# Kernel tuning notes

Hardware: AMD Instinct MI355X
Metric: run time of the kernel (lower is better)

## Reference

```python
import jax, jax.numpy as jnp
import numpy as np

EMB_DIM = 300
VOCAB_X = 50000
VOCAB_Y = 50000
LEN_X = 64
LEN_Y = 64
BATCH = 1024
PAD_ID = 0


def setup_inputs() -> dict:
    key = jax.random.key(0)
    k1, k2, k3, k4, k5, k6, k7 = jax.random.split(key, 7)
    initrange = 0.5 / EMB_DIM
    emb_x = jax.random.uniform(k1, (VOCAB_X, EMB_DIM), jnp.float32, -initrange, initrange)
    emb_y = jax.random.uniform(k2, (VOCAB_Y, EMB_DIM), jnp.float32, -initrange, initrange)
    # padding row zeroed as in init_emb
    emb_x = emb_x.at[PAD_ID].set(0.0)
    emb_y = emb_y.at[PAD_ID].set(0.0)
    return {
        "samp_hid": jax.random.normal(k3, (BATCH, EMB_DIM), jnp.float32),
        "batch_x": jax.random.randint(k4, (BATCH, LEN_X), 0, VOCAB_X, jnp.int64 if jax.config.jax_enable_x64 else jnp.int32),
        "batch_y": jax.random.randint(k5, (BATCH, LEN_Y), 0, VOCAB_Y, jnp.int64 if jax.config.jax_enable_x64 else jnp.int32),
        "emb_x": emb_x,
        "emb_y": emb_y,
        "bias_x": jax.random.uniform(k6, (VOCAB_X,), jnp.float32),
        "bias_y": jax.random.uniform(k7, (VOCAB_Y,), jnp.float32),
    }


def _cal_nll(z, tokens, emb, bias):
    # logits shared across all positions: [B, V]
    logits = z @ emb.T + bias
    logp = jax.nn.log_softmax(logits, axis=-1)            # compute log-softmax ONCE per row
    tok_logp = jnp.take_along_axis(logp, tokens, axis=1)  # [B, L] gather per-position targets
    mask = (tokens != PAD_ID).astype(logits.dtype)        # CrossEntropyLoss(ignore_index=0)
    return jnp.sum(-tok_logp * mask, axis=1)              # sum over positions -> [B]


def reference(samp_hid, batch_x, batch_y, emb_x, emb_y, bias_x, bias_y):
    nll_x = _cal_nll(samp_hid, batch_x, emb_x, bias_x)
    nll_y = _cal_nll(samp_hid, batch_y, emb_y, bias_y)
    return jnp.mean(nll_x + nll_y)
```

## Files before the change

kernel.cpp:

```cpp
#include <hip/hip_runtime.h>

#define V_VOCAB 50000
#define K_DIM   300
#define NROWS   1024
#define LEN     64
#define NBC     98
#define CGS     784
#define KS      19

typedef __attribute__((ext_vector_type(8)))  short bf16x8;
typedef __attribute__((ext_vector_type(16))) float f32x16;

static __device__ __forceinline__ unsigned short f2bf(float f) {
    unsigned int u = __builtin_bit_cast(unsigned int, f);
    u = u + 0x7fffu + ((u >> 16) & 1u);
    return (unsigned short)(u >> 16);
}

static __device__ __forceinline__ f32x16 zero16() {
    f32x16 z;
#pragma unroll
    for (int i = 0; i < 16; ++i) z[i] = 0.0f;
    return z;
}

__global__ void zbf_kernel(const float* __restrict__ z, unsigned short* __restrict__ zbf) {
    int t = blockIdx.x * 256 + threadIdx.x;
    int l    = t & 63;
    int rest = t >> 6;
    int ks   = rest % KS;
    int rblk = rest / KS;
    int row  = rblk * 32 + (l & 31);
    int k0   = ks * 16 + (l >> 5) * 8;
    unsigned short o[8];
#pragma unroll
    for (int j = 0; j < 8; ++j) {
        int k = k0 + j;
        float v = (k < K_DIM) ? z[row * K_DIM + k] : ((k == K_DIM) ? 1.0f : 0.0f);
        o[j] = f2bf(v);
    }
    ushort4* p = (ushort4*)(zbf + (size_t)t * 8);
    p[0] = make_ushort4(o[0], o[1], o[2], o[3]);
    p[1] = make_ushort4(o[4], o[5], o[6], o[7]);
}

__launch_bounds__(512, 2)
__global__ void gemm_kernel(const unsigned short* __restrict__ zbf,
                            const float* __restrict__ emb_x,
                            const float* __restrict__ emb_y,
                            const float* __restrict__ bias_x,
                            const float* __restrict__ bias_y,
                            float* __restrict__ partial) {
    __shared__ unsigned short Zs[2][19456];

    const int tid  = threadIdx.x;
    const int lane = tid & 63;
    const int w    = tid >> 6;
    const int side = blockIdx.y;
    const int bc   = blockIdx.x;
    const float* eg = side ? emb_y : emb_x;
    const float* bg = side ? bias_y : bias_x;
    const int c0 = bc * 512 + w * 64;

    bf16x8 a[2][KS];
#pragma unroll
    for (int cb = 0; cb < 2; ++cb) {
        const int c = c0 + cb * 32 + (lane & 31);
        const bool cv = (c < V_VOCAB);
        const float* erow = eg + (size_t)c * K_DIM;
        const int khi = (lane >> 5) * 8;
#pragma unroll
        for (int ks = 0; ks < KS; ++ks) {
            const int k0 = ks * 16 + khi;
            float f[8];
            if (k0 + 8 <= K_DIM) {
                float4 u  = cv ? *(const float4*)(erow + k0)     : make_float4(0, 0, 0, 0);
                float4 v2 = cv ? *(const float4*)(erow + k0 + 4) : make_float4(0, 0, 0, 0);
                f[0] = u.x;  f[1] = u.y;  f[2] = u.z;  f[3] = u.w;
                f[4] = v2.x; f[5] = v2.y; f[6] = v2.z; f[7] = v2.w;
            } else {
#pragma unroll
                for (int j = 0; j < 8; ++j) {
                    int k = k0 + j;
                    f[j] = (k < K_DIM) ? (cv ? erow[k] : 0.0f)
                         : (k == K_DIM ? (cv ? bg[c] : -3e38f) : 0.0f);
                }
            }
            bf16x8 t;
#pragma unroll
            for (int j = 0; j < 8; ++j) t[j] = (short)f2bf(f[j]);
            a[cb][ks] = t;
        }
    }

    const int cg = (side * NBC + bc) * 8 + w;
    float* pout = partial + (size_t)cg * NROWS;

    uint4 st[5];
    {
        const uint4* src = (const uint4*)zbf;
#pragma unroll
        for (int i = 0; i < 5; ++i) { int idx = i * 512 + tid; if (idx < 2432) st[i] = src[idx]; }
        uint4* dst = (uint4*)&Zs[0][0];
#pragma unroll
        for (int i = 0; i < 5; ++i) { int idx = i * 512 + tid; if (idx < 2432) dst[i * 512 + tid] = st[i]; }
    }
    __syncthreads();

    int buf = 0;
    for (int p = 0; p < 16; ++p) {
        if (p < 15) {
            const uint4* src = (const uint4*)(zbf + (size_t)(p + 1) * 19456);
#pragma unroll
            for (int i = 0; i < 5; ++i) { int idx = i * 512 + tid; if (idx < 2432) st[i] = src[idx]; }
        }

        const unsigned short* zb = &Zs[buf][0];
        f32x16 acc00 = zero16(), acc01 = zero16(), acc10 = zero16(), acc11 = zero16();
#pragma unroll
        for (int ks = 0; ks < KS; ++ks) {
            bf16x8 b0 = *(const bf16x8*)(zb + ((size_t)ks * 64 + lane) * 8);
            bf16x8 b1 = *(const bf16x8*)(zb + ((size_t)(KS + ks) * 64 + lane) * 8);
            acc00 = __builtin_amdgcn_mfma_f32_32x32x16_bf16(a[0][ks], b0, acc00, 0, 0, 0);
            acc01 = __builtin_amdgcn_mfma_f32_32x32x16_bf16(a[0][ks], b1, acc01, 0, 0, 0);
            acc10 = __builtin_amdgcn_mfma_f32_32x32x16_bf16(a[1][ks], b0, acc10, 0, 0, 0);
            acc11 = __builtin_amdgcn_mfma_f32_32x32x16_bf16(a[1][ks], b1, acc11, 0, 0, 0);
        }

        float s0 = 0.0f, s1 = 0.0f;
#pragma unroll
        for (int r = 0; r < 16; ++r) {
            s0 += __expf(acc00[r]) + __expf(acc10[r]);
            s1 += __expf(acc01[r]) + __expf(acc11[r]);
        }
        float t0 = s0 + __shfl_xor(s0, 32, 64);
        float t1 = s1 + __shfl_xor(s1, 32, 64);
        pout[p * 64 + lane] = (lane < 32) ? t0 : t1;

        if (p < 15) {
            uint4* dst = (uint4*)&Zs[buf ^ 1][0];
#pragma unroll
            for (int i = 0; i < 5; ++i) { int idx = i * 512 + tid; if (idx < 2432) dst[i * 512 + tid] = st[i]; }
        }
        __syncthreads();
        buf ^= 1;
    }
}

__global__ void lse_kernel(const float* __restrict__ partial, float* __restrict__ lse) {
    __shared__ float r4[4];
    int bx = blockIdx.x;
    int side = bx >> 10, m = bx & 1023;
    const float* p = partial + (size_t)side * CGS * NROWS + m;
    float s = 0.0f;
    for (int i = threadIdx.x; i < CGS; i += 256) s += p[(size_t)i * NROWS];
#pragma unroll
    for (int off = 32; off > 0; off >>= 1) s += __shfl_xor(s, off, 64);
    if ((threadIdx.x & 63) == 0) r4[threadIdx.x >> 6] = s;
    __syncthreads();
    if (threadIdx.x == 0) lse[bx] = logf(r4[0] + r4[1] + r4[2] + r4[3]);
}

__global__ void gatherdot_kernel(const float* __restrict__ z,
                                 const int* __restrict__ tok_x, const int* __restrict__ tok_y,
                                 const float* __restrict__ emb_x, const float* __restrict__ emb_y,
                                 const float* __restrict__ bias_x, const float* __restrict__ bias_y,
                                 const float* __restrict__ lse, float* __restrict__ nllpart) {
    __shared__ float gs[304];
    const int b = blockIdx.x, side = blockIdx.y, tid = threadIdx.x;
    const int* tokp = (side ? tok_y : tok_x) + b * LEN;
    const float* eg = side ? emb_y : emb_x;
    if (tid < K_DIM) {
        float g0 = 0.0f, g1 = 0.0f;
#pragma unroll 2
        for (int pos = 0; pos < LEN; pos += 2) {
            int t0 = tokp[pos], t1 = tokp[pos + 1];
            if (t0) g0 += eg[(size_t)t0 * K_DIM + tid];
            if (t1) g1 += eg[(size_t)t1 * K_DIM + tid];
        }
        gs[tid] = g0 + g1;
    }
    __syncthreads();
    if (tid < 64) {
        const float* bg = side ? bias_y : bias_x;
        float dp = 0.0f;
#pragma unroll
        for (int i = 0; i < 5; ++i) {
            int d = tid + i * 64;
            if (d < K_DIM) dp += z[(size_t)b * K_DIM + d] * gs[d];
        }
        int t = tokp[tid];
        float bs = t ? bg[t] : 0.0f;
        float ct = t ? 1.0f : 0.0f;
#pragma unroll
        for (int off = 32; off > 0; off >>= 1) {
            dp += __shfl_xor(dp, off, 64);
            bs += __shfl_xor(bs, off, 64);
            ct += __shfl_xor(ct, off, 64);
        }
        if (tid == 0) nllpart[side * NROWS + b] = ct * lse[side * NROWS + b] - dp - bs;
    }
}

__global__ void finalize_kernel(const float* __restrict__ nllpart, float* __restrict__ out) {
    __shared__ float r16[16];
    int i = threadIdx.x;
    float v = nllpart[i] + nllpart[NROWS + i];
#pragma unroll
    for (int off = 32; off > 0; off >>= 1) v += __shfl_xor(v, off, 64);
    if ((i & 63) == 0) r16[i >> 6] = v;
    __syncthreads();
    if (i < 64) {
        float x = (i < 16) ? r16[i] : 0.0f;
#pragma unroll
        for (int off = 8; off > 0; off >>= 1) x += __shfl_xor(x, off, 64);
        if (i == 0) out[0] = x * (1.0f / 1024.0f);
    }
}

extern "C" void kernel_launch(void* const* d_in, const int* in_sizes, int n_in,
                              void* d_out, int out_size, void* d_ws, size_t ws_size,
                              hipStream_t stream) {
    const float* z      = (const float*)d_in[0];
    const int*   tok_x  = (const int*)d_in[1];
    const int*   tok_y  = (const int*)d_in[2];
    const float* emb_x  = (const float*)d_in[3];
    const float* emb_y  = (const float*)d_in[4];
    const float* bias_x = (const float*)d_in[5];
    const float* bias_y = (const float*)d_in[6];
    float* out = (float*)d_out;

    char* ws = (char*)d_ws;
    unsigned short* zbf = (unsigned short*)ws;
    float* partial      = (float*)(ws + 622592);
    float* lse          = (float*)(ws + 622592 + 6422528);
    float* nllpart      = (float*)(ws + 622592 + 6422528 + 8192);
    zbf_kernel<<<152, 256, 0, stream>>>(z, zbf);
    gemm_kernel<<<dim3(NBC, 2), 512, 0, stream>>>(zbf, emb_x, emb_y, bias_x, bias_y, partial);
    lse_kernel<<<2048, 256, 0, stream>>>(partial, lse);
    gatherdot_kernel<<<dim3(NROWS, 2), 320, 0, stream>>>(z, tok_x, tok_y, emb_x, emb_y,
                                                         bias_x, bias_y, lse, nllpart);
    finalize_kernel<<<1, 1024, 0, stream>>>(nllpart, out);
}
```

Baseline: 191.4 us.

## Stream Z tiles via direct global-to-LDS loads with smaller blocks and coalesced LSE

The GEMM kernel now uses 256-thread blocks over 196 column blocks instead of 512 threads over 98, which doubles the grid. The Z tile double buffer is filled with global_load_lds DMA instead of staging through registers, with manual vmcnt waits and raw barriers. The first tile is issued before the embedding fragments load so the two overlap. The LSE reduction is rewritten so each thread sums one row over column groups, giving coalesced reads of the partial matrix across 32 blocks. The risk is fragile hand-tuned waitcnt ordering, and the 32-block LSE launch uses little parallelism.

Measured after the change: 225.1 us. 1.18x slower.

```diff
diff --git a/kernel.cpp b/kernel.cpp
--- a/kernel.cpp
+++ b/kernel.cpp
@@ -4,7 +4,7 @@
 #define K_DIM   300
 #define NROWS   1024
 #define LEN     64
-#define NBC     98
+#define NBC     196
 #define CGS     784
 #define KS      19
 
@@ -22,6 +22,11 @@
 #pragma unroll
     for (int i = 0; i < 16; ++i) z[i] = 0.0f;
     return z;
+}
+
+static __device__ __forceinline__ void gload_lds16(const void* g, void* l) {
+    __builtin_amdgcn_global_load_lds((const __attribute__((address_space(1))) void*)g,
+                                     (__attribute__((address_space(3))) void*)l, 16, 0, 0);
 }
 
 __global__ void zbf_kernel(const float* __restrict__ z, unsigned short* __restrict__ zbf) {
@@ -44,7 +49,7 @@
     p[1] = make_ushort4(o[4], o[5], o[6], o[7]);
 }
 
-__launch_bounds__(512, 2)
+__launch_bounds__(256, 2)
 __global__ void gemm_kernel(const unsigned short* __restrict__ zbf,
                             const float* __restrict__ emb_x,
                             const float* __restrict__ emb_y,
@@ -60,7 +65,17 @@
     const int bc   = blockIdx.x;
     const float* eg = side ? emb_y : emb_x;
     const float* bg = side ? bias_y : bias_x;
-    const int c0 = bc * 512 + w * 64;
+    const int c0 = bc * 256 + w * 64;
+
+    {
+        const unsigned short* src = zbf;
+#pragma unroll
+        for (int i = 0; i < 10; ++i) {
+            int qb = i * 256 + w * 64;
+            if (qb + 64 > 2432) qb = 1024 + w * 64;
+            gload_lds16(src + (size_t)(qb + lane) * 8, &Zs[0][qb * 8]);
+        }
+    }
 
     bf16x8 a[2][KS];
 #pragma unroll
@@ -93,27 +108,25 @@
         }
     }
 
-    const int cg = (side * NBC + bc) * 8 + w;
+    const int cg = (side * NBC + bc) * 4 + w;
     float* pout = partial + (size_t)cg * NROWS;
-
-    uint4 st[5];
-    {
-        const uint4* src = (const uint4*)zbf;
-#pragma unroll
-        for (int i = 0; i < 5; ++i) { int idx = i * 512 + tid; if (idx < 2432) st[i] = src[idx]; }
-        uint4* dst = (uint4*)&Zs[0][0];
-#pragma unroll
-        for (int i = 0; i < 5; ++i) { int idx = i * 512 + tid; if (idx < 2432) dst[i * 512 + tid] = st[i]; }
-    }
-    __syncthreads();
 
     int buf = 0;
     for (int p = 0; p < 16; ++p) {
         if (p < 15) {
-            const uint4* src = (const uint4*)(zbf + (size_t)(p + 1) * 19456);
-#pragma unroll
-            for (int i = 0; i < 5; ++i) { int idx = i * 512 + tid; if (idx < 2432) st[i] = src[idx]; }
-        }
+            const unsigned short* src = zbf + (size_t)(p + 1) * 19456;
+#pragma unroll
+            for (int i = 0; i < 10; ++i) {
+                int qb = i * 256 + w * 64;
+                if (qb + 64 > 2432) qb = 1024 + w * 64;
+                gload_lds16(src + (size_t)(qb + lane) * 8, &Zs[buf ^ 1][qb * 8]);
+            }
+            asm volatile("s_waitcnt vmcnt(10)" ::: "memory");
+        } else {
+            asm volatile("s_waitcnt vmcnt(0)" ::: "memory");
+        }
+        __builtin_amdgcn_s_barrier();
+        __builtin_amdgcn_sched_barrier(0);
 
         const unsigned short* zb = &Zs[buf][0];
         f32x16 acc00 = zero16(), acc01 = zero16(), acc10 = zero16(), acc11 = zero16();
@@ -137,28 +150,28 @@
         float t1 = s1 + __shfl_xor(s1, 32, 64);
         pout[p * 64 + lane] = (lane < 32) ? t0 : t1;
 
-        if (p < 15) {
-            uint4* dst = (uint4*)&Zs[buf ^ 1][0];
-#pragma unroll
-            for (int i = 0; i < 5; ++i) { int idx = i * 512 + tid; if (idx < 2432) dst[i * 512 + tid] = st[i]; }
-        }
-        __syncthreads();
+        __builtin_amdgcn_s_barrier();
         buf ^= 1;
     }
 }
 
 __global__ void lse_kernel(const float* __restrict__ partial, float* __restrict__ lse) {
-    __shared__ float r4[4];
-    int bx = blockIdx.x;
-    int side = bx >> 10, m = bx & 1023;
-    const float* p = partial + (size_t)side * CGS * NROWS + m;
+    __shared__ float red[256];
+    int side = blockIdx.x >> 4;
+    int mg   = blockIdx.x & 15;
+    int m    = mg * 64 + (threadIdx.x & 63);
+    int sg   = threadIdx.x >> 6;
+    const float* p = partial + (size_t)side * CGS * NROWS;
     float s = 0.0f;
-    for (int i = threadIdx.x; i < CGS; i += 256) s += p[(size_t)i * NROWS];
-#pragma unroll
-    for (int off = 32; off > 0; off >>= 1) s += __shfl_xor(s, off, 64);
-    if ((threadIdx.x & 63) == 0) r4[threadIdx.x >> 6] = s;
+    for (int cg = sg; cg < CGS; cg += 4)
+        s += p[(size_t)cg * NROWS + m];
+    red[threadIdx.x] = s;
     __syncthreads();
-    if (threadIdx.x == 0) lse[bx] = logf(r4[0] + r4[1] + r4[2] + r4[3]);
+    if (threadIdx.x < 64) {
+        float t = red[threadIdx.x] + red[64 + threadIdx.x]
+                + red[128 + threadIdx.x] + red[192 + threadIdx.x];
+        lse[side * NROWS + mg * 64 + threadIdx.x] = logf(t);
+    }
 }
 
 __global__ void gatherdot_kernel(const float* __restrict__ z,
@@ -236,8 +249,8 @@
     float* lse          = (float*)(ws + 622592 + 6422528);
     float* nllpart      = (float*)(ws + 622592 + 6422528 + 8192);
     zbf_kernel<<<152, 256, 0, stream>>>(z, zbf);
-    gemm_kernel<<<dim3(NBC, 2), 512, 0, stream>>>(zbf, emb_x, emb_y, bias_x, bias_y, partial);
-    lse_kernel<<<2048, 256, 0, stream>>>(partial, lse);
+    gemm_kernel<<<dim3(NBC, 2), 256, 0, stream>>>(zbf, emb_x, emb_y, bias_x, bias_y, partial);
+    lse_kernel<<<32, 256, 0, stream>>>(partial, lse);
     gatherdot_kernel<<<dim3(NROWS, 2), 320, 0, stream>>>(z, tok_x, tok_y, emb_x, emb_y,
                                                          bias_x, bias_y, lse, nllpart);
     finalize_kernel<<<1, 1024, 0, stream>>>(nllpart, out);
```
